# Kernel tuning notes

Measured on AMD Instinct MI355X. Metric: run time of the kernel, lower is better.

## Reference

```python
import jax, jax.numpy as jnp
import numpy as np
import math

NUM_LANDMARKS = 64
HEAD_DIM = 64
NUM_HEAD = 16
BATCH = 4
SEQ_LEN = 4096


def iterative_inv(mat, n_iter=6):
    # mat: [..., m, m]
    I = jnp.eye(mat.shape[-1], dtype=mat.dtype)
    K = mat
    # scalar normalization: global max of column sums * global max of row sums
    scale = 1.0 / (jnp.max(jnp.sum(jnp.abs(K), axis=-2)) * jnp.max(jnp.sum(jnp.abs(K), axis=-1)))
    V = scale * jnp.swapaxes(K, -1, -2)
    for _ in range(n_iter):
        KV = jnp.matmul(K, V)
        V = jnp.matmul(0.25 * V, 13.0 * I - jnp.matmul(KV, 15.0 * I - jnp.matmul(KV, 7.0 * I - KV)))
    return V


def setup_inputs() -> dict:
    key = jax.random.key(0)
    k1, k2, k3 = jax.random.split(key, 3)
    shape = (BATCH, NUM_HEAD, SEQ_LEN, HEAD_DIM)
    Q = jax.random.normal(k1, shape, dtype=jnp.float32)
    K = jax.random.normal(k2, shape, dtype=jnp.float32)
    V = jax.random.normal(k3, shape, dtype=jnp.float32)
    return {"Q": Q, "K": K, "V": V}


def reference(Q, K, V):
    seq_len = Q.shape[-2]
    m = NUM_LANDMARKS
    scale = 1.0 / math.sqrt(math.sqrt(HEAD_DIM))
    Q = Q * scale
    K = K * scale
    # landmark pooling: mean over contiguous segments of length seq_len // m
    seg = seq_len // m
    Q_lm = Q.reshape(-1, NUM_HEAD, m, seg, HEAD_DIM).mean(axis=-2)  # [B,H,m,d]
    K_lm = K.reshape(-1, NUM_HEAD, m, seg, HEAD_DIM).mean(axis=-2)  # [B,H,m,d]
    # three softmax kernels
    kernel_1 = jax.nn.softmax(jnp.einsum('bhsd,bhmd->bhsm', Q, K_lm), axis=-1)   # [B,H,S,m]
    kernel_2 = jax.nn.softmax(jnp.einsum('bhmd,bhnd->bhmn', Q_lm, K_lm), axis=-1)  # [B,H,m,m]
    kernel_3 = jax.nn.softmax(jnp.einsum('bhmd,bhsd->bhms', Q_lm, K), axis=-1)   # [B,H,m,S]
    inv_k2 = iterative_inv(kernel_2)
    X = jnp.matmul(jnp.matmul(kernel_1, inv_k2), jnp.matmul(kernel_3, V))  # [B,H,S,d]
    return X
```

## Files before the change

### kernel.cpp

```cpp
#include <hip/hip_runtime.h>
#include <hip/hip_bf16.h>

#define KP  72
#define SCALE 0.35355339059327379f

typedef __attribute__((ext_vector_type(8))) short bf16x8;
typedef __attribute__((ext_vector_type(4))) float f32x4;
#define MFMA_BF16 __builtin_amdgcn_mfma_f32_16x16x32_bf16

__device__ __forceinline__ short f2b(float f) {
    unsigned u = __float_as_uint(f);
    u += 0x7fff + ((u >> 16) & 1);
    return (short)(u >> 16);
}
__device__ __forceinline__ float b2f(short h) {
    return __uint_as_float(((unsigned)(unsigned short)h) << 16);
}

__device__ __forceinline__ int SWI(int row, int colS) {
    return (((row << 7) + (colS << 1)) ^ ((row & 7) << 4)) >> 1;
}

__global__ __launch_bounds__(256) void pool_kernel(const float* __restrict__ Q,
                                                   const float* __restrict__ K,
                                                   short* __restrict__ Qlm_bh,
                                                   short* __restrict__ Qlm_bl,
                                                   short* __restrict__ Klm_bh,
                                                   short* __restrict__ Klm_bl) {
    __shared__ float4 red[256];
    const int blk = blockIdx.x;
    const int t = threadIdx.x;
    const int d4 = t & 15;
    const int rg = t >> 4;
    const float4* Q4 = reinterpret_cast<const float4*>(Q);
    const float4* K4 = reinterpret_cast<const float4*>(K);

    float4 sQ = {0.f, 0.f, 0.f, 0.f}, sK = {0.f, 0.f, 0.f, 0.f};
#pragma unroll
    for (int rr = 0; rr < 4; rr++) {
        int row = blk * 64 + rg * 4 + rr;
        int off4 = (row << 4) + d4;
        float4 q = Q4[off4], k = K4[off4];
        sQ.x += q.x; sQ.y += q.y; sQ.z += q.z; sQ.w += q.w;
        sK.x += k.x; sK.y += k.y; sK.z += k.z; sK.w += k.w;
    }
    const float c = SCALE * (1.0f / 64.0f);
    red[t] = sQ;
    __syncthreads();
    if (t < 16) {
        float4 s = {0.f, 0.f, 0.f, 0.f};
#pragma unroll
        for (int g = 0; g < 16; g++) {
            float4 v = red[g * 16 + t];
            s.x += v.x; s.y += v.y; s.z += v.z; s.w += v.w;
        }
        s.x *= c; s.y *= c; s.z *= c; s.w *= c;
        short h0 = f2b(s.x), h1 = f2b(s.y), h2 = f2b(s.z), h3 = f2b(s.w);
        ushort4 uh = {(unsigned short)h0, (unsigned short)h1,
                      (unsigned short)h2, (unsigned short)h3};
        ushort4 ul = {(unsigned short)f2b(s.x - b2f(h0)), (unsigned short)f2b(s.y - b2f(h1)),
                      (unsigned short)f2b(s.z - b2f(h2)), (unsigned short)f2b(s.w - b2f(h3))};
        *reinterpret_cast<ushort4*>(&Qlm_bh[blk * 64 + t * 4]) = uh;
        *reinterpret_cast<ushort4*>(&Qlm_bl[blk * 64 + t * 4]) = ul;
    }
    __syncthreads();
    red[t] = sK;
    __syncthreads();
    if (t < 16) {
        float4 s = {0.f, 0.f, 0.f, 0.f};
#pragma unroll
        for (int g = 0; g < 16; g++) {
            float4 v = red[g * 16 + t];
            s.x += v.x; s.y += v.y; s.z += v.z; s.w += v.w;
        }
        s.x *= c; s.y *= c; s.z *= c; s.w *= c;
        short h0 = f2b(s.x), h1 = f2b(s.y), h2 = f2b(s.z), h3 = f2b(s.w);
        ushort4 uh = {(unsigned short)h0, (unsigned short)h1,
                      (unsigned short)h2, (unsigned short)h3};
        ushort4 ul = {(unsigned short)f2b(s.x - b2f(h0)), (unsigned short)f2b(s.y - b2f(h1)),
                      (unsigned short)f2b(s.z - b2f(h2)), (unsigned short)f2b(s.w - b2f(h3))};
        *reinterpret_cast<ushort4*>(&Klm_bh[blk * 64 + t * 4]) = uh;
        *reinterpret_cast<ushort4*>(&Klm_bl[blk * 64 + t * 4]) = ul;
    }
}

__global__ __launch_bounds__(256) void k2_kernel(const short* __restrict__ Qlm_bh,
                                                 const short* __restrict__ Qlm_bl,
                                                 const short* __restrict__ Klm_bh,
                                                 const short* __restrict__ Klm_bl,
                                                 float* __restrict__ K2g,
                                                 unsigned* __restrict__ colmax) {
    __shared__ float csum[16 * 64];
    const int bh = blockIdx.x, t = threadIdx.x;
    const int w = t >> 6, lane = t & 63, quad = lane >> 4, l15 = lane & 15;

    const bf16x8* Ah = reinterpret_cast<const bf16x8*>(Qlm_bh + bh * 4096);
    const bf16x8* Al = reinterpret_cast<const bf16x8*>(Qlm_bl + bh * 4096);
    const bf16x8* Bh = reinterpret_cast<const bf16x8*>(Klm_bh + bh * 4096);
    const bf16x8* Bl = reinterpret_cast<const bf16x8*>(Klm_bl + bh * 4096);
    bf16x8 ah0 = Ah[(w * 16 + l15) * 8 + quad], ah1 = Ah[(w * 16 + l15) * 8 + quad + 4];
    bf16x8 al0 = Al[(w * 16 + l15) * 8 + quad], al1 = Al[(w * 16 + l15) * 8 + quad + 4];

    f32x4 c[4];
#pragma unroll
    for (int nt = 0; nt < 4; nt++) {
        bf16x8 bh0 = Bh[(nt * 16 + l15) * 8 + quad], bh1 = Bh[(nt * 16 + l15) * 8 + quad + 4];
        bf16x8 bl0 = Bl[(nt * 16 + l15) * 8 + quad], bl1 = Bl[(nt * 16 + l15) * 8 + quad + 4];
        f32x4 cc = {0.f, 0.f, 0.f, 0.f};
        cc = MFMA_BF16(ah0, bh0, cc, 0, 0, 0); cc = MFMA_BF16(ah1, bh1, cc, 0, 0, 0);
        cc = MFMA_BF16(ah0, bl0, cc, 0, 0, 0); cc = MFMA_BF16(ah1, bl1, cc, 0, 0, 0);
        cc = MFMA_BF16(al0, bh0, cc, 0, 0, 0); cc = MFMA_BF16(al1, bh1, cc, 0, 0, 0);
        c[nt] = cc;
    }
    float m[4] = {-1e30f, -1e30f, -1e30f, -1e30f};
#pragma unroll
    for (int nt = 0; nt < 4; nt++)
#pragma unroll
        for (int reg = 0; reg < 4; reg++) m[reg] = fmaxf(m[reg], c[nt][reg]);
#pragma unroll
    for (int reg = 0; reg < 4; reg++) {
        float v = m[reg];
        v = fmaxf(v, __shfl_xor(v, 1)); v = fmaxf(v, __shfl_xor(v, 2));
        v = fmaxf(v, __shfl_xor(v, 4)); v = fmaxf(v, __shfl_xor(v, 8));
        m[reg] = v;
    }
    float e[4][4];
    float rs[4] = {0.f, 0.f, 0.f, 0.f};
#pragma unroll
    for (int nt = 0; nt < 4; nt++)
#pragma unroll
        for (int reg = 0; reg < 4; reg++) {
            float ev = __expf(c[nt][reg] - m[reg]);
            e[nt][reg] = ev; rs[reg] += ev;
        }
#pragma unroll
    for (int reg = 0; reg < 4; reg++) {
        float v = rs[reg];
        v += __shfl_xor(v, 1); v += __shfl_xor(v, 2);
        v += __shfl_xor(v, 4); v += __shfl_xor(v, 8);
        rs[reg] = 1.0f / v;
    }
    float ps[4] = {0.f, 0.f, 0.f, 0.f};
#pragma unroll
    for (int nt = 0; nt < 4; nt++) {
#pragma unroll
        for (int reg = 0; reg < 4; reg++) {
            float p = e[nt][reg] * rs[reg];
            K2g[bh * 4096 + (w * 16 + quad * 4 + reg) * 64 + nt * 16 + l15] = p;
            ps[nt] += p;
        }
        csum[(w * 4 + quad) * 64 + nt * 16 + l15] = ps[nt];
    }
    __syncthreads();
    if (t < 64) {
        float s = 0.f;
#pragma unroll
        for (int i = 0; i < 16; i++) s += csum[i * 64 + t];
        atomicMax(colmax, __float_as_uint(s));
    }
}

__global__ __launch_bounds__(256) void fused_inv_k3v(const short* __restrict__ Qlm_bh,
                                                     const float* __restrict__ K,
                                                     const float* __restrict__ V,
                                                     float* __restrict__ W2acc,
                                                     float* __restrict__ rowsum3,
                                                     const float* __restrict__ K2g,
                                                     const unsigned* __restrict__ colmax,
                                                     float* __restrict__ K2invg) {
    __shared__ __align__(16) char smem[65536];
    const int t = threadIdx.x;
    const int w = t >> 6, lane = t & 63, quad = lane >> 4, l15 = lane & 15;

    if (blockIdx.x < 64) {
        short* Krh = reinterpret_cast<short*>(smem);
        short* Krl = Krh + 4096;
        short* Ath = Krl + 4096;
        short* Atl = Ath + 4096;
        short* B1h = Atl + 4096;
        short* B1l = B1h + 4096;
        short* B2h = B1l + 4096;
        short* B2l = B2h + 4096;
        const int bh = blockIdx.x;
        const float scv = 1.0f / __uint_as_float(*colmax);
        const float* Kg = K2g + bh * 4096;

#pragma unroll
        for (int n = 0; n < 4; n++) {
            int f4 = t + n * 256;
            int r = f4 >> 4, c0 = (f4 & 15) * 4;
            float4 kk = *reinterpret_cast<const float4*>(Kg + r * 64 + c0);
            short h0 = f2b(kk.x), h1 = f2b(kk.y), h2 = f2b(kk.z), h3 = f2b(kk.w);
            ushort4 uh = {(unsigned short)h0, (unsigned short)h1,
                          (unsigned short)h2, (unsigned short)h3};
            ushort4 ul = {(unsigned short)f2b(kk.x - b2f(h0)), (unsigned short)f2b(kk.y - b2f(h1)),
                          (unsigned short)f2b(kk.z - b2f(h2)), (unsigned short)f2b(kk.w - b2f(h3))};
            *reinterpret_cast<ushort4*>(&Krh[SWI(r, c0)]) = uh;
            *reinterpret_cast<ushort4*>(&Krl[SWI(r, c0)]) = ul;
            float s0 = scv * kk.x, s1 = scv * kk.y, s2 = scv * kk.z, s3 = scv * kk.w;
            short g0 = f2b(s0), g1 = f2b(s1), g2 = f2b(s2), g3 = f2b(s3);
            ushort4 vh = {(unsigned short)g0, (unsigned short)g1,
                          (unsigned short)g2, (unsigned short)g3};
            ushort4 vl = {(unsigned short)f2b(s0 - b2f(g0)), (unsigned short)f2b(s1 - b2f(g1)),
                          (unsigned short)f2b(s2 - b2f(g2)), (unsigned short)f2b(s3 - b2f(g3))};
            *reinterpret_cast<ushort4*>(&B1h[SWI(r, c0)]) = vh;
            *reinterpret_cast<ushort4*>(&B1l[SWI(r, c0)]) = vl;
            float t0 = scv * Kg[(c0 + 0) * 64 + r];
            float t1 = scv * Kg[(c0 + 1) * 64 + r];
            float t2 = scv * Kg[(c0 + 2) * 64 + r];
            float t3 = scv * Kg[(c0 + 3) * 64 + r];
            short e0 = f2b(t0), e1 = f2b(t1), e2 = f2b(t2), e3 = f2b(t3);
            ushort4 th = {(unsigned short)e0, (unsigned short)e1,
                          (unsigned short)e2, (unsigned short)e3};
            ushort4 tl = {(unsigned short)f2b(t0 - b2f(e0)), (unsigned short)f2b(t1 - b2f(e1)),
                          (unsigned short)f2b(t2 - b2f(e2)), (unsigned short)f2b(t3 - b2f(e3))};
            *reinterpret_cast<ushort4*>(&B2h[SWI(r, c0)]) = th;
            *reinterpret_cast<ushort4*>(&B2l[SWI(r, c0)]) = tl;
        }
        float vreg[4][4];
#pragma unroll
        for (int nt = 0; nt < 4; nt++) {
            float4 vv = *reinterpret_cast<const float4*>(
                Kg + (nt * 16 + l15) * 64 + w * 16 + quad * 4);
            vreg[nt][0] = scv * vv.x; vreg[nt][1] = scv * vv.y;
            vreg[nt][2] = scv * vv.z; vreg[nt][3] = scv * vv.w;
        }
        __syncthreads();

#define LOADA(Lh, Ll) \
        bf16x8 ah0 = *reinterpret_cast<const bf16x8*>(&Lh[SWI(w * 16 + l15, quad * 8)]); \
        bf16x8 ah1 = *reinterpret_cast<const bf16x8*>(&Lh[SWI(w * 16 + l15, quad * 8 + 32)]); \
        bf16x8 al0 = *reinterpret_cast<const bf16x8*>(&Ll[SWI(w * 16 + l15, quad * 8)]); \
        bf16x8 al1 = *reinterpret_cast<const bf16x8*>(&Ll[SWI(w * 16 + l15, quad * 8 + 32)]);
#define PRODNT(Bh, Bl, nt, c) { \
        bf16x8 bh0 = *reinterpret_cast<const bf16x8*>(&Bh[SWI(nt * 16 + l15, quad * 8)]); \
        bf16x8 bh1 = *reinterpret_cast<const bf16x8*>(&Bh[SWI(nt * 16 + l15, quad * 8 + 32)]); \
        bf16x8 bl0 = *reinterpret_cast<const bf16x8*>(&Bl[SWI(nt * 16 + l15, quad * 8)]); \
        bf16x8 bl1 = *reinterpret_cast<const bf16x8*>(&Bl[SWI(nt * 16 + l15, quad * 8 + 32)]); \
        c = MFMA_BF16(ah0, bh0, c, 0, 0, 0); c = MFMA_BF16(ah1, bh1, c, 0, 0, 0); \
        c = MFMA_BF16(ah0, bl0, c, 0, 0, 0); c = MFMA_BF16(ah1, bl1, c, 0, 0, 0); \
        c = MFMA_BF16(al0, bh0, c, 0, 0, 0); c = MFMA_BF16(al1, bh1, c, 0, 0, 0); \
        c = MFMA_BF16(al0, bl0, c, 0, 0, 0); c = MFMA_BF16(al1, bl1, c, 0, 0, 0); }

        for (int iter = 0; iter < 6; iter++) {
            {
                LOADA(Krh, Krl)
#pragma unroll
                for (int nt = 0; nt < 4; nt++) {
                    f32x4 c = {0.f, 0.f, 0.f, 0.f};
                    PRODNT(B1h, B1l, nt, c)
                    short h0 = f2b(c[0]), h1 = f2b(c[1]), h2 = f2b(c[2]), h3 = f2b(c[3]);
                    ushort4 uh = {(unsigned short)h0, (unsigned short)h1,
                                  (unsigned short)h2, (unsigned short)h3};
                    ushort4 ul = {(unsigned short)f2b(c[0] - b2f(h0)),
                                  (unsigned short)f2b(c[1] - b2f(h1)),
                                  (unsigned short)f2b(c[2] - b2f(h2)),
                                  (unsigned short)f2b(c[3] - b2f(h3))};
                    *reinterpret_cast<ushort4*>(&Ath[SWI(nt * 16 + l15, w * 16 + quad * 4)]) = uh;
                    *reinterpret_cast<ushort4*>(&Atl[SWI(nt * 16 + l15, w * 16 + quad * 4)]) = ul;
                }
            }
            __syncthreads();
            float p[4][4];
            {
                LOADA(B2h, B2l)
#pragma unroll
                for (int nt = 0; nt < 4; nt++) {
                    f32x4 c = {0.f, 0.f, 0.f, 0.f};
                    PRODNT(Ath, Atl, nt, c)
#pragma unroll
                    for (int reg = 0; reg < 4; reg++) {
                        p[nt][reg] = c[reg];
                        short hh = f2b(c[reg]);
                        B1h[SWI(w * 16 + quad * 4 + reg, nt * 16 + l15)] = hh;
                        B1l[SWI(w * 16 + quad * 4 + reg, nt * 16 + l15)] = f2b(c[reg] - b2f(hh));
                    }
                }
            }
            __syncthreads();
            float q[4][4];
            {
                LOADA(B1h, B1l)
#pragma unroll
                for (int nt = 0; nt < 4; nt++) {
                    f32x4 c = {0.f, 0.f, 0.f, 0.f};
                    PRODNT(Ath, Atl, nt, c)
#pragma unroll
                    for (int reg = 0; reg < 4; reg++) {
                        q[nt][reg] = c[reg];
                        short hh = f2b(c[reg]);
                        B2h[SWI(w * 16 + quad * 4 + reg, nt * 16 + l15)] = hh;
                        B2l[SWI(w * 16 + quad * 4 + reg, nt * 16 + l15)] = f2b(c[reg] - b2f(hh));
                    }
                }
            }
            __syncthreads();
            {
                LOADA(B2h, B2l)
#pragma unroll
                for (int nt = 0; nt < 4; nt++) {
                    f32x4 c = {0.f, 0.f, 0.f, 0.f};
                    PRODNT(Ath, Atl, nt, c)
#pragma unroll
                    for (int reg = 0; reg < 4; reg++)
                        vreg[nt][reg] = 0.25f * (13.f * vreg[nt][reg] - 15.f * p[nt][reg]
                                                 + 7.f * q[nt][reg] - c[reg]);
                }
            }
#pragma unroll
            for (int nt = 0; nt < 4; nt++) {
                short h0 = f2b(vreg[nt][0]), h1 = f2b(vreg[nt][1]);
                short h2 = f2b(vreg[nt][2]), h3 = f2b(vreg[nt][3]);
                short g0 = f2b(vreg[nt][0] - b2f(h0)), g1 = f2b(vreg[nt][1] - b2f(h1));
                short g2 = f2b(vreg[nt][2] - b2f(h2)), g3 = f2b(vreg[nt][3] - b2f(h3));
                ushort4 uh = {(unsigned short)h0, (unsigned short)h1,
                              (unsigned short)h2, (unsigned short)h3};
                ushort4 ul = {(unsigned short)g0, (unsigned short)g1,
                              (unsigned short)g2, (unsigned short)g3};
                *reinterpret_cast<ushort4*>(&B1h[SWI(nt * 16 + l15, w * 16 + quad * 4)]) = uh;
                *reinterpret_cast<ushort4*>(&B1l[SWI(nt * 16 + l15, w * 16 + quad * 4)]) = ul;
                B2h[SWI(w * 16 + quad * 4 + 0, nt * 16 + l15)] = h0;
                B2h[SWI(w * 16 + quad * 4 + 1, nt * 16 + l15)] = h1;
                B2h[SWI(w * 16 + quad * 4 + 2, nt * 16 + l15)] = h2;
                B2h[SWI(w * 16 + quad * 4 + 3, nt * 16 + l15)] = h3;
                B2l[SWI(w * 16 + quad * 4 + 0, nt * 16 + l15)] = g0;
                B2l[SWI(w * 16 + quad * 4 + 1, nt * 16 + l15)] = g1;
                B2l[SWI(w * 16 + quad * 4 + 2, nt * 16 + l15)] = g2;
                B2l[SWI(w * 16 + quad * 4 + 3, nt * 16 + l15)] = g3;
            }
            __syncthreads();
        }
#undef LOADA
#undef PRODNT
#pragma unroll
        for (int nt = 0; nt < 4; nt++)
#pragma unroll
            for (int reg = 0; reg < 4; reg++)
                K2invg[bh * 4096 + (w * 16 + quad * 4 + reg) * 64 + nt * 16 + l15] =
                    vreg[nt][reg];
        return;
    }

    short* Kt = reinterpret_cast<short*>(smem);
    short* Vt = Kt + 64 * KP;
    short* Eb = Vt + 64 * KP;
    const int idx = blockIdx.x - 64;
    const int chunk = idx & 31, bh = idx >> 5;
    const float4* K4 = reinterpret_cast<const float4*>(K);
    const float4* V4 = reinterpret_cast<const float4*>(V);
    const int dg = t & 15;
    const int kr = t >> 4;
    const int bhBase = bh * 4096;

    const bf16x8* Qb = reinterpret_cast<const bf16x8*>(Qlm_bh + bh * 4096);
    bf16x8 a0 = Qb[(w * 16 + l15) * 8 + quad];
    bf16x8 a1 = Qb[(w * 16 + l15) * 8 + quad + 4];

    f32x4 oacc[4];
    float rsum[4];
#pragma unroll
    for (int nt = 0; nt < 4; nt++) { oacc[nt] = (f32x4){0.f, 0.f, 0.f, 0.f}; rsum[nt] = 0.f; }

    const int sb0 = chunk * 128;
    for (int tile = 0; tile < 2; tile++) {
        const int sb = sb0 + tile * 64;
        __syncthreads();
#pragma unroll
        for (int n = 0; n < 4; n++) {
            float4 kk = K4[(bhBase + sb + kr + 16 * n) * 16 + dg];
            ushort4 uk = { (unsigned short)f2b(SCALE * kk.x), (unsigned short)f2b(SCALE * kk.y),
                           (unsigned short)f2b(SCALE * kk.z), (unsigned short)f2b(SCALE * kk.w) };
            *reinterpret_cast<ushort4*>(&Kt[(kr + 16 * n) * KP + dg * 4]) = uk;
        }
        {
            float4 pv0 = V4[(bhBase + sb + kr * 4 + 0) * 16 + dg];
            float4 pv1 = V4[(bhBase + sb + kr * 4 + 1) * 16 + dg];
            float4 pv2 = V4[(bhBase + sb + kr * 4 + 2) * 16 + dg];
            float4 pv3 = V4[(bhBase + sb + kr * 4 + 3) * 16 + dg];
            ushort4 u0 = { (unsigned short)f2b(pv0.x), (unsigned short)f2b(pv1.x),
                           (unsigned short)f2b(pv2.x), (unsigned short)f2b(pv3.x) };
            ushort4 u1 = { (unsigned short)f2b(pv0.y), (unsigned short)f2b(pv1.y),
                           (unsigned short)f2b(pv2.y), (unsigned short)f2b(pv3.y) };
            ushort4 u2 = { (unsigned short)f2b(pv0.z), (unsigned short)f2b(pv1.z),
                           (unsigned short)f2b(pv2.z), (unsigned short)f2b(pv3.z) };
            ushort4 u3 = { (unsigned short)f2b(pv0.w), (unsigned short)f2b(pv1.w),
                           (unsigned short)f2b(pv2.w), (unsigned short)f2b(pv3.w) };
            *reinterpret_cast<ushort4*>(&Vt[(dg * 4 + 0) * KP + kr * 4]) = u0;
            *reinterpret_cast<ushort4*>(&Vt[(dg * 4 + 1) * KP + kr * 4]) = u1;
            *reinterpret_cast<ushort4*>(&Vt[(dg * 4 + 2) * KP + kr * 4]) = u2;
            *reinterpret_cast<ushort4*>(&Vt[(dg * 4 + 3) * KP + kr * 4]) = u3;
        }
        __syncthreads();
#pragma unroll
        for (int nt = 0; nt < 4; nt++) {
            bf16x8 b0 = *reinterpret_cast<const bf16x8*>(&Kt[(nt * 16 + l15) * KP + quad * 8]);
            bf16x8 b1 = *reinterpret_cast<const bf16x8*>(&Kt[(nt * 16 + l15) * KP + quad * 8 + 32]);
            f32x4 c = {0.f, 0.f, 0.f, 0.f};
            c = MFMA_BF16(a0, b0, c, 0, 0, 0);
            c = MFMA_BF16(a1, b1, c, 0, 0, 0);
#pragma unroll
            for (int reg = 0; reg < 4; reg++) {
                float e = __expf(c[reg]);
                rsum[reg] += e;
                Eb[(w * 16 + quad * 4 + reg) * KP + nt * 16 + l15] = f2b(e);
            }
        }
        bf16x8 e0 = *reinterpret_cast<const bf16x8*>(&Eb[(w * 16 + l15) * KP + quad * 8]);
        bf16x8 e1 = *reinterpret_cast<const bf16x8*>(&Eb[(w * 16 + l15) * KP + quad * 8 + 32]);
#pragma unroll
        for (int nt = 0; nt < 4; nt++) {
            bf16x8 b0 = *reinterpret_cast<const bf16x8*>(&Vt[(nt * 16 + l15) * KP + quad * 8]);
            bf16x8 b1 = *reinterpret_cast<const bf16x8*>(&Vt[(nt * 16 + l15) * KP + quad * 8 + 32]);
            oacc[nt] = MFMA_BF16(e0, b0, oacc[nt], 0, 0, 0);
            oacc[nt] = MFMA_BF16(e1, b1, oacc[nt], 0, 0, 0);
        }
    }
#pragma unroll
    for (int reg = 0; reg < 4; reg++) {
        float s = rsum[reg];
        s += __shfl_xor(s, 1); s += __shfl_xor(s, 2);
        s += __shfl_xor(s, 4); s += __shfl_xor(s, 8);
        rsum[reg] = s;
    }
    const int row0 = w * 16 + quad * 4;
    if (l15 == 0) {
#pragma unroll
        for (int reg = 0; reg < 4; reg++)
            atomicAdd(&rowsum3[bh * 64 + row0 + reg], rsum[reg]);
    }
#pragma unroll
    for (int nt = 0; nt < 4; nt++)
#pragma unroll
        for (int reg = 0; reg < 4; reg++)
            atomicAdd(&W2acc[(bh * 64 + row0 + reg) * 64 + nt * 16 + l15], oacc[nt][reg]);
}

__global__ __launch_bounds__(256) void wmid_kernel(const float* __restrict__ K2invg,
                                                   const float* __restrict__ W2acc,
                                                   const float* __restrict__ rowsum3,
                                                   short* __restrict__ Wth,
                                                   short* __restrict__ Wtl) {
    __shared__ short W2th[4096], W2tl[4096];
    const int bh = blockIdx.x, t = threadIdx.x;
    const int w = t >> 6, lane = t & 63, quad = lane >> 4, l15 = lane & 15;

#pragma unroll
    for (int n16 = 0; n16 < 16; n16++) {
        int f = t + n16 * 256;
        int k = f >> 6, n = f & 63;
        float v = W2acc[bh * 4096 + k * 64 + n] / rowsum3[bh * 64 + k];
        short hi = f2b(v);
        W2th[SWI(n, k)] = hi;
        W2tl[SWI(n, k)] = f2b(v - b2f(hi));
    }
    const float* Ar = K2invg + bh * 4096 + (w * 16 + l15) * 64;
    float4 x0 = *reinterpret_cast<const float4*>(Ar + quad * 8);
    float4 x1 = *reinterpret_cast<const float4*>(Ar + quad * 8 + 4);
    float4 x2 = *reinterpret_cast<const float4*>(Ar + quad * 8 + 32);
    float4 x3 = *reinterpret_cast<const float4*>(Ar + quad * 8 + 36);
    bf16x8 ah0, al0, ah1, al1;
    {
        float a[8] = {x0.x, x0.y, x0.z, x0.w, x1.x, x1.y, x1.z, x1.w};
        float b[8] = {x2.x, x2.y, x2.z, x2.w, x3.x, x3.y, x3.z, x3.w};
#pragma unroll
        for (int i = 0; i < 8; i++) {
            short h = f2b(a[i]); ah0[i] = h; al0[i] = f2b(a[i] - b2f(h));
            short g = f2b(b[i]); ah1[i] = g; al1[i] = f2b(b[i] - b2f(g));
        }
    }
    __syncthreads();
#pragma unroll
    for (int nt = 0; nt < 4; nt++) {
        bf16x8 bh0 = *reinterpret_cast<const bf16x8*>(&W2th[SWI(nt * 16 + l15, quad * 8)]);
        bf16x8 bh1 = *reinterpret_cast<const bf16x8*>(&W2th[SWI(nt * 16 + l15, quad * 8 + 32)]);
        bf16x8 bl0 = *reinterpret_cast<const bf16x8*>(&W2tl[SWI(nt * 16 + l15, quad * 8)]);
        bf16x8 bl1 = *reinterpret_cast<const bf16x8*>(&W2tl[SWI(nt * 16 + l15, quad * 8 + 32)]);
        f32x4 cc = {0.f, 0.f, 0.f, 0.f};
        cc = MFMA_BF16(ah0, bh0, cc, 0, 0, 0); cc = MFMA_BF16(ah1, bh1, cc, 0, 0, 0);
        cc = MFMA_BF16(ah0, bl0, cc, 0, 0, 0); cc = MFMA_BF16(ah1, bl1, cc, 0, 0, 0);
        cc = MFMA_BF16(al0, bh0, cc, 0, 0, 0); cc = MFMA_BF16(al1, bh1, cc, 0, 0, 0);
#pragma unroll
        for (int reg = 0; reg < 4; reg++) {
            float wv = cc[reg];
            short hi = f2b(wv);
            int col = nt * 16 + l15, r = w * 16 + quad * 4 + reg;
            Wth[bh * 4096 + col * 64 + r] = hi;
            Wtl[bh * 4096 + col * 64 + r] = f2b(wv - b2f(hi));
        }
    }
}

__global__ __launch_bounds__(256, 4) void final_mfma(const float* __restrict__ Q,
                                                     const short* __restrict__ Klm_b,
                                                     const short* __restrict__ Wth,
                                                     const short* __restrict__ Wtl,
                                                     float* __restrict__ out) {
    __shared__ short Eb[64 * KP];
    const int sc = blockIdx.x, bh = blockIdx.y, t = threadIdx.x;
    const int w = t >> 6, lane = t & 63, quad = lane >> 4, l15 = lane & 15;
    const int row = w * 16 + l15;

    const bf16x8* Kb = reinterpret_cast<const bf16x8*>(Klm_b + bh * 4096);
    bf16x8 kb[4][2];
#pragma unroll
    for (int nt = 0; nt < 4; nt++) {
        kb[nt][0] = Kb[(nt * 16 + l15) * 8 + quad];
        kb[nt][1] = Kb[(nt * 16 + l15) * 8 + quad + 4];
    }
    const bf16x8* Hb = reinterpret_cast<const bf16x8*>(Wth + bh * 4096);
    const bf16x8* Lb = reinterpret_cast<const bf16x8*>(Wtl + bh * 4096);

    const size_t qbase = ((size_t)bh * 4096 + sc * 256 + row) * 64 + quad * 8;
    float4 qa = *reinterpret_cast<const float4*>(Q + qbase);
    float4 qb = *reinterpret_cast<const float4*>(Q + qbase + 4);
    float4 qc = *reinterpret_cast<const float4*>(Q + qbase + 32);
    float4 qd = *reinterpret_cast<const float4*>(Q + qbase + 36);

#pragma unroll
    for (int st = 0; st < 4; st++) {
        bf16x8 a0, a1;
        a0[0] = f2b(SCALE * qa.x); a0[1] = f2b(SCALE * qa.y);
        a0[2] = f2b(SCALE * qa.z); a0[3] = f2b(SCALE * qa.w);
        a0[4] = f2b(SCALE * qb.x); a0[5] = f2b(SCALE * qb.y);
        a0[6] = f2b(SCALE * qb.z); a0[7] = f2b(SCALE * qb.w);
        a1[0] = f2b(SCALE * qc.x); a1[1] = f2b(SCALE * qc.y);
        a1[2] = f2b(SCALE * qc.z); a1[3] = f2b(SCALE * qc.w);
        a1[4] = f2b(SCALE * qd.x); a1[5] = f2b(SCALE * qd.y);
        a1[6] = f2b(SCALE * qd.z); a1[7] = f2b(SCALE * qd.w);
        if (st < 3) {
            const float* np = Q + qbase + (size_t)(st + 1) * 4096;
            qa = *reinterpret_cast<const float4*>(np);
            qb = *reinterpret_cast<const float4*>(np + 4);
            qc = *reinterpret_cast<const float4*>(np + 32);
            qd = *reinterpret_cast<const float4*>(np + 36);
        }
        float rsum[4] = {0.f, 0.f, 0.f, 0.f};
#pragma unroll
        for (int nt = 0; nt < 4; nt++) {
            f32x4 c = {0.f, 0.f, 0.f, 0.f};
            c = MFMA_BF16(a0, kb[nt][0], c, 0, 0, 0);
            c = MFMA_BF16(a1, kb[nt][1], c, 0, 0, 0);
#pragma unroll
            for (int reg = 0; reg < 4; reg++) {
                float e = __expf(c[reg]);
                rsum[reg] += e;
                Eb[(w * 16 + quad * 4 + reg) * KP + nt * 16 + l15] = f2b(e);
            }
        }
#pragma unroll
        for (int reg = 0; reg < 4; reg++) {
            float s = rsum[reg];
            s += __shfl_xor(s, 1); s += __shfl_xor(s, 2);
            s += __shfl_xor(s, 4); s += __shfl_xor(s, 8);
            rsum[reg] = 1.0f / s;
        }
        bf16x8 e0 = *reinterpret_cast<const bf16x8*>(&Eb[row * KP + quad * 8]);
        bf16x8 e1 = *reinterpret_cast<const bf16x8*>(&Eb[row * KP + quad * 8 + 32]);
        const int row0 = w * 16 + quad * 4;
        const int s0 = sc * 256 + st * 64;
#pragma unroll
        for (int nt = 0; nt < 4; nt++) {
            bf16x8 bh0 = Hb[(nt * 16 + l15) * 8 + quad];
            bf16x8 bh1 = Hb[(nt * 16 + l15) * 8 + quad + 4];
            bf16x8 bl0 = Lb[(nt * 16 + l15) * 8 + quad];
            bf16x8 bl1 = Lb[(nt * 16 + l15) * 8 + quad + 4];
            f32x4 c = {0.f, 0.f, 0.f, 0.f};
            c = MFMA_BF16(e0, bh0, c, 0, 0, 0);
            c = MFMA_BF16(e1, bh1, c, 0, 0, 0);
            c = MFMA_BF16(e0, bl0, c, 0, 0, 0);
            c = MFMA_BF16(e1, bl1, c, 0, 0, 0);
#pragma unroll
            for (int reg = 0; reg < 4; reg++)
                out[((size_t)bh * 4096 + s0 + row0 + reg) * 64 + nt * 16 + l15] =
                    c[reg] * rsum[reg];
        }
    }
}

extern "C" void kernel_launch(void* const* d_in, const int* in_sizes, int n_in,
                              void* d_out, int out_size, void* d_ws, size_t ws_size,
                              hipStream_t stream) {
    const float* Q = (const float*)d_in[0];
    const float* K = (const float*)d_in[1];
    const float* V = (const float*)d_in[2];
    float* out = (float*)d_out;
    float* ws = (float*)d_ws;

    float* K2      = ws;
    float* K2inv   = ws + 262144;
    float* W2acc   = ws + 524288;
    float* rowsum3 = ws + 786432;
    unsigned* colmax = (unsigned*)(ws + 790528);
    short* Qlm_bh  = (short*)(ws + 790532);
    short* Qlm_bl  = Qlm_bh + 262144;
    short* Klm_bh  = Qlm_bl + 262144;
    short* Klm_bl  = Klm_bh + 262144;
    short* Wth     = Klm_bl + 262144;
    short* Wtl     = Wth + 262144;

    hipMemsetAsync(W2acc, 0, (262144 + 4096 + 1) * sizeof(float), stream);

    pool_kernel<<<4096, 256, 0, stream>>>(Q, K, Qlm_bh, Qlm_bl, Klm_bh, Klm_bl);
    k2_kernel<<<64, 256, 0, stream>>>(Qlm_bh, Qlm_bl, Klm_bh, Klm_bl, K2, colmax);
    fused_inv_k3v<<<2112, 256, 0, stream>>>(Qlm_bh, K, V, W2acc, rowsum3, K2, colmax, K2inv);
    wmid_kernel<<<64, 256, 0, stream>>>(K2inv, W2acc, rowsum3, Wth, Wtl);
    final_mfma<<<dim3(16, 64), 256, 0, stream>>>(Q, Klm_bh, Wth, Wtl, out);
}
```

Before: 299.5 us.

## Fold memset into pool kernel, keep K in registers, halve k3v blocks, pipeline Q loads

Drops the separate hipMemsetAsync by zeroing the accumulator buffer inside pool_kernel, and keeps the inverse's K operand in registers instead of shared memory, which shrinks LDS to 48KB and removes two barriers per iteration. It also halves the number of k3v blocks by giving each block four 64-row tiles instead of two, and double-buffers Q loads in final_mfma. The risks are racing the zeroing against colmax if ordering is wrong, higher register pressure, and fewer blocks to spread across CUs.

```diff
diff --git a/kernel.cpp b/kernel.cpp
--- a/kernel.cpp
+++ b/kernel.cpp
@@ -26,7 +26,9 @@
                                                    short* __restrict__ Qlm_bh,
                                                    short* __restrict__ Qlm_bl,
                                                    short* __restrict__ Klm_bh,
-                                                   short* __restrict__ Klm_bl) {
+                                                   short* __restrict__ Klm_bl,
+                                                   float* __restrict__ zeroBuf,
+                                                   int zeroCount) {
     __shared__ float4 red[256];
     const int blk = blockIdx.x;
     const int t = threadIdx.x;
@@ -34,6 +36,9 @@
     const int rg = t >> 4;
     const float4* Q4 = reinterpret_cast<const float4*>(Q);
     const float4* K4 = reinterpret_cast<const float4*>(K);
+
+    int zi = blk * 256 + t;
+    if (zi < zeroCount) zeroBuf[zi] = 0.f;
 
     float4 sQ = {0.f, 0.f, 0.f, 0.f}, sK = {0.f, 0.f, 0.f, 0.f};
 #pragma unroll
@@ -168,14 +173,12 @@
                                                      const float* __restrict__ K2g,
                                                      const unsigned* __restrict__ colmax,
                                                      float* __restrict__ K2invg) {
-    __shared__ __align__(16) char smem[65536];
+    __shared__ __align__(16) char smem[49152];
     const int t = threadIdx.x;
     const int w = t >> 6, lane = t & 63, quad = lane >> 4, l15 = lane & 15;
 
     if (blockIdx.x < 64) {
-        short* Krh = reinterpret_cast<short*>(smem);
-        short* Krl = Krh + 4096;
-        short* Ath = Krl + 4096;
+        short* Ath = reinterpret_cast<short*>(smem);
         short* Atl = Ath + 4096;
         short* B1h = Atl + 4096;
         short* B1l = B1h + 4096;
@@ -185,18 +188,26 @@
         const float scv = 1.0f / __uint_as_float(*colmax);
         const float* Kg = K2g + bh * 4096;
 
+        bf16x8 kh0, kl0, kh1, kl1;
+        {
+            const float* Kr = Kg + (w * 16 + l15) * 64;
+            float4 x0 = *reinterpret_cast<const float4*>(Kr + quad * 8);
+            float4 x1 = *reinterpret_cast<const float4*>(Kr + quad * 8 + 4);
+            float4 x2 = *reinterpret_cast<const float4*>(Kr + quad * 8 + 32);
+            float4 x3 = *reinterpret_cast<const float4*>(Kr + quad * 8 + 36);
+            float a[8] = {x0.x, x0.y, x0.z, x0.w, x1.x, x1.y, x1.z, x1.w};
+            float b[8] = {x2.x, x2.y, x2.z, x2.w, x3.x, x3.y, x3.z, x3.w};
+#pragma unroll
+            for (int i = 0; i < 8; i++) {
+                short h = f2b(a[i]); kh0[i] = h; kl0[i] = f2b(a[i] - b2f(h));
+                short g = f2b(b[i]); kh1[i] = g; kl1[i] = f2b(b[i] - b2f(g));
+            }
+        }
 #pragma unroll
         for (int n = 0; n < 4; n++) {
             int f4 = t + n * 256;
             int r = f4 >> 4, c0 = (f4 & 15) * 4;
             float4 kk = *reinterpret_cast<const float4*>(Kg + r * 64 + c0);
-            short h0 = f2b(kk.x), h1 = f2b(kk.y), h2 = f2b(kk.z), h3 = f2b(kk.w);
-            ushort4 uh = {(unsigned short)h0, (unsigned short)h1,
-                          (unsigned short)h2, (unsigned short)h3};
-            ushort4 ul = {(unsigned short)f2b(kk.x - b2f(h0)), (unsigned short)f2b(kk.y - b2f(h1)),
-                          (unsigned short)f2b(kk.z - b2f(h2)), (unsigned short)f2b(kk.w - b2f(h3))};
-            *reinterpret_cast<ushort4*>(&Krh[SWI(r, c0)]) = uh;
-            *reinterpret_cast<ushort4*>(&Krl[SWI(r, c0)]) = ul;
             float s0 = scv * kk.x, s1 = scv * kk.y, s2 = scv * kk.z, s3 = scv * kk.w;
             short g0 = f2b(s0), g1 = f2b(s1), g2 = f2b(s2), g3 = f2b(s3);
             ushort4 vh = {(unsigned short)g0, (unsigned short)g1,
@@ -232,33 +243,30 @@
         bf16x8 ah1 = *reinterpret_cast<const bf16x8*>(&Lh[SWI(w * 16 + l15, quad * 8 + 32)]); \
         bf16x8 al0 = *reinterpret_cast<const bf16x8*>(&Ll[SWI(w * 16 + l15, quad * 8)]); \
         bf16x8 al1 = *reinterpret_cast<const bf16x8*>(&Ll[SWI(w * 16 + l15, quad * 8 + 32)]);
-#define PRODNT(Bh, Bl, nt, c) { \
+#define PROD8(AH0, AH1, AL0, AL1, Bh, Bl, nt, c) { \
         bf16x8 bh0 = *reinterpret_cast<const bf16x8*>(&Bh[SWI(nt * 16 + l15, quad * 8)]); \
         bf16x8 bh1 = *reinterpret_cast<const bf16x8*>(&Bh[SWI(nt * 16 + l15, quad * 8 + 32)]); \
         bf16x8 bl0 = *reinterpret_cast<const bf16x8*>(&Bl[SWI(nt * 16 + l15, quad * 8)]); \
         bf16x8 bl1 = *reinterpret_cast<const bf16x8*>(&Bl[SWI(nt * 16 + l15, quad * 8 + 32)]); \
-        c = MFMA_BF16(ah0, bh0, c, 0, 0, 0); c = MFMA_BF16(ah1, bh1, c, 0, 0, 0); \
-        c = MFMA_BF16(ah0, bl0, c, 0, 0, 0); c = MFMA_BF16(ah1, bl1, c, 0, 0, 0); \
-        c = MFMA_BF16(al0, bh0, c, 0, 0, 0); c = MFMA_BF16(al1, bh1, c, 0, 0, 0); \
-        c = MFMA_BF16(al0, bl0, c, 0, 0, 0); c = MFMA_BF16(al1, bl1, c, 0, 0, 0); }
+        c = MFMA_BF16(AH0, bh0, c, 0, 0, 0); c = MFMA_BF16(AH1, bh1, c, 0, 0, 0); \
+        c = MFMA_BF16(AH0, bl0, c, 0, 0, 0); c = MFMA_BF16(AH1, bl1, c, 0, 0, 0); \
+        c = MFMA_BF16(AL0, bh0, c, 0, 0, 0); c = MFMA_BF16(AL1, bh1, c, 0, 0, 0); \
+        c = MFMA_BF16(AL0, bl0, c, 0, 0, 0); c = MFMA_BF16(AL1, bl1, c, 0, 0, 0); }
 
         for (int iter = 0; iter < 6; iter++) {
-            {
-                LOADA(Krh, Krl)
-#pragma unroll
-                for (int nt = 0; nt < 4; nt++) {
-                    f32x4 c = {0.f, 0.f, 0.f, 0.f};
-                    PRODNT(B1h, B1l, nt, c)
-                    short h0 = f2b(c[0]), h1 = f2b(c[1]), h2 = f2b(c[2]), h3 = f2b(c[3]);
-                    ushort4 uh = {(unsigned short)h0, (unsigned short)h1,
-                                  (unsigned short)h2, (unsigned short)h3};
-                    ushort4 ul = {(unsigned short)f2b(c[0] - b2f(h0)),
-                                  (unsigned short)f2b(c[1] - b2f(h1)),
-                                  (unsigned short)f2b(c[2] - b2f(h2)),
-                                  (unsigned short)f2b(c[3] - b2f(h3))};
-                    *reinterpret_cast<ushort4*>(&Ath[SWI(nt * 16 + l15, w * 16 + quad * 4)]) = uh;
-                    *reinterpret_cast<ushort4*>(&Atl[SWI(nt * 16 + l15, w * 16 + quad * 4)]) = ul;
-                }
+#pragma unroll
+            for (int nt = 0; nt < 4; nt++) {
+                f32x4 c = {0.f, 0.f, 0.f, 0.f};
+                PROD8(kh0, kh1, kl0, kl1, B1h, B1l, nt, c)
+                short h0 = f2b(c[0]), h1 = f2b(c[1]), h2 = f2b(c[2]), h3 = f2b(c[3]);
+                ushort4 uh = {(unsigned short)h0, (unsigned short)h1,
+                              (unsigned short)h2, (unsigned short)h3};
+                ushort4 ul = {(unsigned short)f2b(c[0] - b2f(h0)),
+                              (unsigned short)f2b(c[1] - b2f(h1)),
+                              (unsigned short)f2b(c[2] - b2f(h2)),
+                              (unsigned short)f2b(c[3] - b2f(h3))};
+                *reinterpret_cast<ushort4*>(&Ath[SWI(nt * 16 + l15, w * 16 + quad * 4)]) = uh;
+                *reinterpret_cast<ushort4*>(&Atl[SWI(nt * 16 + l15, w * 16 + quad * 4)]) = ul;
             }
             __syncthreads();
             float p[4][4];
@@ -267,7 +275,7 @@
 #pragma unroll
                 for (int nt = 0; nt < 4; nt++) {
                     f32x4 c = {0.f, 0.f, 0.f, 0.f};
-                    PRODNT(Ath, Atl, nt, c)
+                    PROD8(ah0, ah1, al0, al1, Ath, Atl, nt, c)
 #pragma unroll
                     for (int reg = 0; reg < 4; reg++) {
                         p[nt][reg] = c[reg];
@@ -277,14 +285,13 @@
                     }
                 }
             }
-            __syncthreads();
             float q[4][4];
             {
                 LOADA(B1h, B1l)
 #pragma unroll
                 for (int nt = 0; nt < 4; nt++) {
                     f32x4 c = {0.f, 0.f, 0.f, 0.f};
-                    PRODNT(Ath, Atl, nt, c)
+                    PROD8(ah0, ah1, al0, al1, Ath, Atl, nt, c)
 #pragma unroll
                     for (int reg = 0; reg < 4; reg++) {
                         q[nt][reg] = c[reg];
@@ -294,19 +301,19 @@
                     }
                 }
             }
-            __syncthreads();
             {
                 LOADA(B2h, B2l)
 #pragma unroll
                 for (int nt = 0; nt < 4; nt++) {
                     f32x4 c = {0.f, 0.f, 0.f, 0.f};
-                    PRODNT(Ath, Atl, nt, c)
+                    PROD8(ah0, ah1, al0, al1, Ath, Atl, nt, c)
 #pragma unroll
                     for (int reg = 0; reg < 4; reg++)
                         vreg[nt][reg] = 0.25f * (13.f * vreg[nt][reg] - 15.f * p[nt][reg]
                                                  + 7.f * q[nt][reg] - c[reg]);
                 }
             }
+            __syncthreads();
 #pragma unroll
             for (int nt = 0; nt < 4; nt++) {
                 short h0 = f2b(vreg[nt][0]), h1 = f2b(vreg[nt][1]);
@@ -331,7 +338,7 @@
             __syncthreads();
         }
 #undef LOADA
-#undef PRODNT
+#undef PROD8
 #pragma unroll
         for (int nt = 0; nt < 4; nt++)
 #pragma unroll
@@ -345,7 +352,7 @@
     short* Vt = Kt + 64 * KP;
     short* Eb = Vt + 64 * KP;
     const int idx = blockIdx.x - 64;
-    const int chunk = idx & 31, bh = idx >> 5;
+    const int chunk = idx & 15, bh = idx >> 4;
     const float4* K4 = reinterpret_cast<const float4*>(K);
     const float4* V4 = reinterpret_cast<const float4*>(V);
     const int dg = t & 15;
@@ -361,8 +368,8 @@
 #pragma unroll
     for (int nt = 0; nt < 4; nt++) { oacc[nt] = (f32x4){0.f, 0.f, 0.f, 0.f}; rsum[nt] = 0.f; }
 
-    const int sb0 = chunk * 128;
-    for (int tile = 0; tile < 2; tile++) {
+    const int sb0 = chunk * 256;
+    for (int tile = 0; tile < 4; tile++) {
         const int sb = sb0 + tile * 64;
         __syncthreads();
 #pragma unroll
@@ -511,70 +518,76 @@
     const bf16x8* Lb = reinterpret_cast<const bf16x8*>(Wtl + bh * 4096);
 
     const size_t qbase = ((size_t)bh * 4096 + sc * 256 + row) * 64 + quad * 8;
-    float4 qa = *reinterpret_cast<const float4*>(Q + qbase);
-    float4 qb = *reinterpret_cast<const float4*>(Q + qbase + 4);
-    float4 qc = *reinterpret_cast<const float4*>(Q + qbase + 32);
-    float4 qd = *reinterpret_cast<const float4*>(Q + qbase + 36);
-
-#pragma unroll
-    for (int st = 0; st < 4; st++) {
-        bf16x8 a0, a1;
-        a0[0] = f2b(SCALE * qa.x); a0[1] = f2b(SCALE * qa.y);
-        a0[2] = f2b(SCALE * qa.z); a0[3] = f2b(SCALE * qa.w);
-        a0[4] = f2b(SCALE * qb.x); a0[5] = f2b(SCALE * qb.y);
-        a0[6] = f2b(SCALE * qb.z); a0[7] = f2b(SCALE * qb.w);
-        a1[0] = f2b(SCALE * qc.x); a1[1] = f2b(SCALE * qc.y);
-        a1[2] = f2b(SCALE * qc.z); a1[3] = f2b(SCALE * qc.w);
-        a1[4] = f2b(SCALE * qd.x); a1[5] = f2b(SCALE * qd.y);
-        a1[6] = f2b(SCALE * qd.z); a1[7] = f2b(SCALE * qd.w);
-        if (st < 3) {
-            const float* np = Q + qbase + (size_t)(st + 1) * 4096;
-            qa = *reinterpret_cast<const float4*>(np);
-            qb = *reinterpret_cast<const float4*>(np + 4);
-            qc = *reinterpret_cast<const float4*>(np + 32);
-            qd = *reinterpret_cast<const float4*>(np + 36);
-        }
-        float rsum[4] = {0.f, 0.f, 0.f, 0.f};
-#pragma unroll
-        for (int nt = 0; nt < 4; nt++) {
-            f32x4 c = {0.f, 0.f, 0.f, 0.f};
-            c = MFMA_BF16(a0, kb[nt][0], c, 0, 0, 0);
-            c = MFMA_BF16(a1, kb[nt][1], c, 0, 0, 0);
-#pragma unroll
-            for (int reg = 0; reg < 4; reg++) {
-                float e = __expf(c[reg]);
-                rsum[reg] += e;
-                Eb[(w * 16 + quad * 4 + reg) * KP + nt * 16 + l15] = f2b(e);
-            }
-        }
-#pragma unroll
-        for (int reg = 0; reg < 4; reg++) {
-            float s = rsum[reg];
-            s += __shfl_xor(s, 1); s += __shfl_xor(s, 2);
-            s += __shfl_xor(s, 4); s += __shfl_xor(s, 8);
-            rsum[reg] = 1.0f / s;
-        }
-        bf16x8 e0 = *reinterpret_cast<const bf16x8*>(&Eb[row * KP + quad * 8]);
-        bf16x8 e1 = *reinterpret_cast<const bf16x8*>(&Eb[row * KP + quad * 8 + 32]);
-        const int row0 = w * 16 + quad * 4;
-        const int s0 = sc * 256 + st * 64;
-#pragma unroll
-        for (int nt = 0; nt < 4; nt++) {
-            bf16x8 bh0 = Hb[(nt * 16 + l15) * 8 + quad];
-            bf16x8 bh1 = Hb[(nt * 16 + l15) * 8 + quad + 4];
-            bf16x8 bl0 = Lb[(nt * 16 + l15) * 8 + quad];
-            bf16x8 bl1 = Lb[(nt * 16 + l15) * 8 + quad + 4];
-            f32x4 c = {0.f, 0.f, 0.f, 0.f};
-            c = MFMA_BF16(e0, bh0, c, 0, 0, 0);
-            c = MFMA_BF16(e1, bh1, c, 0, 0, 0);
-            c = MFMA_BF16(e0, bl0, c, 0, 0, 0);
-            c = MFMA_BF16(e1, bl1, c, 0, 0, 0);
-#pragma unroll
-            for (int reg = 0; reg < 4; reg++)
-                out[((size_t)bh * 4096 + s0 + row0 + reg) * 64 + nt * 16 + l15] =
-                    c[reg] * rsum[reg];
-        }
-    }
+
+#define FM_LOADQ(p0, p1, p2, p3, stt) { \
+        const float* np = Q + qbase + (size_t)(stt) * 4096; \
+        p0 = *reinterpret_cast<const float4*>(np); \
+        p1 = *reinterpret_cast<const float4*>(np + 4); \
+        p2 = *reinterpret_cast<const float4*>(np + 32); \
+        p3 = *reinterpret_cast<const float4*>(np + 36); }
+
+#define FM_TILE(p0, p1, p2, p3, stt) { \
+        bf16x8 a0, a1; \
+        a0[0] = f2b(SCALE * p0.x); a0[1] = f2b(SCALE * p0.y); \
+        a0[2] = f2b(SCALE * p0.z); a0[3] = f2b(SCALE * p0.w); \
+        a0[4] = f2b(SCALE * p1.x); a0[5] = f2b(SCALE * p1.y); \
+        a0[6] = f2b(SCALE * p1.z); a0[7] = f2b(SCALE * p1.w); \
+        a1[0] = f2b(SCALE * p2.x); a1[1] = f2b(SCALE * p2.y); \
+        a1[2] = f2b(SCALE * p2.z); a1[3] = f2b(SCALE * p2.w); \
+        a1[4] = f2b(SCALE * p3.x); a1[5] = f2b(SCALE * p3.y); \
+        a1[6] = f2b(SCALE * p3.z); a1[7] = f2b(SCALE * p3.w); \
+        float rsum[4] = {0.f, 0.f, 0.f, 0.f}; \
+        _Pragma("unroll") \
+        for (int nt = 0; nt < 4; nt++) { \
+            f32x4 c = {0.f, 0.f, 0.f, 0.f}; \
+            c = MFMA_BF16(a0, kb[nt][0], c, 0, 0, 0); \
+            c = MFMA_BF16(a1, kb[nt][1], c, 0, 0, 0); \
+            _Pragma("unroll") \
+            for (int reg = 0; reg < 4; reg++) { \
+                float e = __expf(c[reg]); \
+                rsum[reg] += e; \
+                Eb[(w * 16 + quad * 4 + reg) * KP + nt * 16 + l15] = f2b(e); \
+            } \
+        } \
+        _Pragma("unroll") \
+        for (int reg = 0; reg < 4; reg++) { \
+            float s = rsum[reg]; \
+            s += __shfl_xor(s, 1); s += __shfl_xor(s, 2); \
+            s += __shfl_xor(s, 4); s += __shfl_xor(s, 8); \
+            rsum[reg] = 1.0f / s; \
+        } \
+        bf16x8 e0 = *reinterpret_cast<const bf16x8*>(&Eb[row * KP + quad * 8]); \
+        bf16x8 e1 = *reinterpret_cast<const bf16x8*>(&Eb[row * KP + quad * 8 + 32]); \
+        const int row0 = w * 16 + quad * 4; \
+        const int s0 = sc * 256 + (stt) * 64; \
+        _Pragma("unroll") \
+        for (int nt = 0; nt < 4; nt++) { \
+            bf16x8 bh0 = Hb[(nt * 16 + l15) * 8 + quad]; \
+            bf16x8 bh1 = Hb[(nt * 16 + l15) * 8 + quad + 4]; \
+            bf16x8 bl0 = Lb[(nt * 16 + l15) * 8 + quad]; \
+            bf16x8 bl1 = Lb[(nt * 16 + l15) * 8 + quad + 4]; \
+            f32x4 c = {0.f, 0.f, 0.f, 0.f}; \
+            c = MFMA_BF16(e0, bh0, c, 0, 0, 0); \
+            c = MFMA_BF16(e1, bh1, c, 0, 0, 0); \
+            c = MFMA_BF16(e0, bl0, c, 0, 0, 0); \
+            c = MFMA_BF16(e1, bl1, c, 0, 0, 0); \
+            _Pragma("unroll") \
+            for (int reg = 0; reg < 4; reg++) \
+                out[((size_t)bh * 4096 + s0 + row0 + reg) * 64 + nt * 16 + l15] = \
+                    c[reg] * rsum[reg]; \
+        } }
+
+    float4 qa0, qa1, qa2, qa3, qb0, qb1, qb2, qb3;
+    FM_LOADQ(qa0, qa1, qa2, qa3, 0)
+    FM_LOADQ(qb0, qb1, qb2, qb3, 1)
+    FM_TILE(qa0, qa1, qa2, qa3, 0)
+    FM_LOADQ(qa0, qa1, qa2, qa3, 2)
+    FM_TILE(qb0, qb1, qb2, qb3, 1)
+    FM_LOADQ(qb0, qb1, qb2, qb3, 3)
+    FM_TILE(qa0, qa1, qa2, qa3, 2)
+    FM_TILE(qb0, qb1, qb2, qb3, 3)
+#undef FM_LOADQ
+#undef FM_TILE
 }
 
 extern "C" void kernel_launch(void* const* d_in, const int* in_sizes, int n_in,
@@ -598,11 +611,10 @@
     short* Wth     = Klm_bl + 262144;
     short* Wtl     = Wth + 262144;
 
-    hipMemsetAsync(W2acc, 0, (262144 + 4096 + 1) * sizeof(float), stream);
-
-    pool_kernel<<<4096, 256, 0, stream>>>(Q, K, Qlm_bh, Qlm_bl, Klm_bh, Klm_bl);
+    pool_kernel<<<4096, 256, 0, stream>>>(Q, K, Qlm_bh, Qlm_bl, Klm_bh, Klm_bl,
+                                          W2acc, 262144 + 4096 + 1);
     k2_kernel<<<64, 256, 0, stream>>>(Qlm_bh, Qlm_bl, Klm_bh, Klm_bl, K2, colmax);
-    fused_inv_k3v<<<2112, 256, 0, stream>>>(Qlm_bh, K, V, W2acc, rowsum3, K2, colmax, K2inv);
+    fused_inv_k3v<<<1088, 256, 0, stream>>>(Qlm_bh, K, V, W2acc, rowsum3, K2, colmax, K2inv);
     wmid_kernel<<<64, 256, 0, stream>>>(K2inv, W2acc, rowsum3, Wth, Wtl);
     final_mfma<<<dim3(16, 64), 256, 0, stream>>>(Q, Klm_bh, Wth, Wtl, out);
 }
```

Measured after the change: 284.6 us. 1.05x faster.
